# Performance work log

Hardware: AMD Instinct MI355X
Metric: run time of the kernel (lower is better)

## Reference

```python
import jax, jax.numpy as jnp
import numpy as np

D_MODEL = 1024
N_HEADS = 16
D_K = D_MODEL // N_HEADS
D_FF = 4096
EPS = 1e-6
NEG = -1e9


def layer_norm(x, alpha, bias):
    # torch: mean/std over last dim, std is unbiased (ddof=1), eps added to std
    mean = jnp.mean(x, axis=-1, keepdims=True)
    std = jnp.std(x, axis=-1, keepdims=True, ddof=1)
    return alpha * (x - mean) / (std + EPS) + bias


def setup_inputs() -> dict:
    key = jax.random.key(0)
    ks = jax.random.split(key, 12)
    B, S = 2, 2048
    s_attn = 1.0 / np.sqrt(D_MODEL)
    s_ff1 = 1.0 / np.sqrt(D_MODEL)
    s_ff2 = 1.0 / np.sqrt(D_FF)
    inp = {
        "x": jax.random.normal(ks[0], (B, S, D_MODEL), jnp.float32),
        "mask": jnp.ones((1, 1, S, S), jnp.int32),
        "wq": jax.random.normal(ks[1], (D_MODEL, D_MODEL), jnp.float32) * s_attn,
        "bq": jnp.zeros((D_MODEL,), jnp.float32),
        "wk": jax.random.normal(ks[2], (D_MODEL, D_MODEL), jnp.float32) * s_attn,
        "bk": jnp.zeros((D_MODEL,), jnp.float32),
        "wv": jax.random.normal(ks[3], (D_MODEL, D_MODEL), jnp.float32) * s_attn,
        "bv": jnp.zeros((D_MODEL,), jnp.float32),
        "wo": jax.random.normal(ks[4], (D_MODEL, D_MODEL), jnp.float32) * s_attn,
        "bo": jnp.zeros((D_MODEL,), jnp.float32),
        "w1": jax.random.normal(ks[5], (D_MODEL, D_FF), jnp.float32) * s_ff1,
        "b1": jnp.zeros((D_FF,), jnp.float32),
        "w2": jax.random.normal(ks[6], (D_FF, D_MODEL), jnp.float32) * s_ff2,
        "b2": jnp.zeros((D_MODEL,), jnp.float32),
        "a1": jnp.ones((1,), jnp.float32),
        "c1": jnp.zeros((1,), jnp.float32),
        "a2": jnp.ones((1,), jnp.float32),
        "c2": jnp.zeros((1,), jnp.float32),
    }
    return inp


def reference(x, mask, wq, bq, wk, bk, wv, bv, wo, bo, w1, b1, w2, b2, a1, c1, a2, c2):
    B, S, D = x.shape

    def mha(h):
        q = (h @ wq + bq).reshape(B, S, N_HEADS, D_K).transpose(0, 2, 1, 3)
        k = (h @ wk + bk).reshape(B, S, N_HEADS, D_K).transpose(0, 2, 1, 3)
        v = (h @ wv + bv).reshape(B, S, N_HEADS, D_K).transpose(0, 2, 1, 3)
        scores = jnp.einsum('bhqd,bhkd->bhqk', q, k) / jnp.sqrt(jnp.float32(D_K))
        scores = jnp.where(mask == 0, jnp.float32(NEG), scores)
        weights = jax.nn.softmax(scores, axis=-1)
        out = jnp.einsum('bhqk,bhkd->bhqd', weights, v)
        out = out.transpose(0, 2, 1, 3).reshape(B, S, D)
        return out @ wo + bo

    def ffn(h):
        return jax.nn.relu(h @ w1 + b1) @ w2 + b2

    # pre-LN residual connections (dropout=0 / eval mode)
    x = x + mha(layer_norm(x, a1, c1))
    x = x + ffn(layer_norm(x, a2, c2))
    return x
```

## Files before the change

### kernel.cpp

```cpp
#include <hip/hip_runtime.h>
#include <hip/hip_bf16.h>
#include <type_traits>


typedef __attribute__((ext_vector_type(8))) short short8v;
typedef __attribute__((ext_vector_type(4))) float f32x4;
typedef __attribute__((ext_vector_type(4))) unsigned uint4v;

#define D_MODEL 1024
#define SEQ 2048
#define NROWS 4096

__device__ __forceinline__ short f2bs(float f) {
  __hip_bfloat16 h = __float2bfloat16(f);
  return __builtin_bit_cast(short, h);
}

__device__ __forceinline__ unsigned cvtpk(float lo, float hi) {
  unsigned r;
  asm("v_cvt_pk_bf16_f32 %0, %1, %2" : "=v"(r) : "v"(lo), "v"(hi));
  return r;
}

__device__ __forceinline__ void perm16swap(unsigned& a, unsigned& b) {
  asm volatile("v_permlane16_swap_b32 %0, %1" : "+v"(a), "+v"(b));
}

__device__ __forceinline__ void async_copy16(const void* g, void* l) {
  __builtin_amdgcn_global_load_lds(
      (__attribute__((address_space(1))) void*)g,
      (__attribute__((address_space(3))) void*)l,
      16, 0, 0);
}

__global__ __launch_bounds__(256)
void transpose_bf16_kernel(const float* __restrict__ in, short* __restrict__ out,
                           int K, int N, float scale) {
  __shared__ float tile[32][33];
  const int n0 = blockIdx.x * 32, k0 = blockIdx.y * 32;
  const int tx = threadIdx.x, ty = threadIdx.y;
#pragma unroll
  for (int j = 0; j < 4; ++j)
    tile[ty + j * 8][tx] = in[(size_t)(k0 + ty + j * 8) * N + n0 + tx];
  __syncthreads();
#pragma unroll
  for (int j = 0; j < 4; ++j)
    out[(size_t)(n0 + ty + j * 8) * K + k0 + tx] = f2bs(tile[tx][ty + j * 8] * scale);
}

__global__ __launch_bounds__(256)
void transpose_v_kernel(const short* __restrict__ qkv, short* __restrict__ vt) {
  __shared__ short tile[32][33];
  const int bh = blockIdx.z, b = bh >> 4, h = bh & 15;
  const int s0 = blockIdx.x * 32, d0 = blockIdx.y * 32;
  const int tx = threadIdx.x, ty = threadIdx.y;
  const short* src = qkv + ((size_t)b * SEQ) * 3072 + 2048 + h * 64;
#pragma unroll
  for (int j = 0; j < 4; ++j)
    tile[ty + j * 8][tx] = src[(size_t)(s0 + ty + j * 8) * 3072 + d0 + tx];
  __syncthreads();
  short* dst = vt + (size_t)bh * 64 * SEQ;
#pragma unroll
  for (int j = 0; j < 4; ++j)
    dst[(size_t)(d0 + ty + j * 8) * SEQ + s0 + tx] = tile[tx][ty + j * 8];
}

__global__ void concat_bias_kernel(const float* __restrict__ bq, const float* __restrict__ bk,
                                   const float* __restrict__ bv, float* __restrict__ outb,
                                   float qscale) {
  int i = blockIdx.x * 256 + threadIdx.x;
  float v = (i < 1024) ? bq[i] * qscale : (i < 2048 ? bk[i - 1024] : bv[i - 2048]);
  outb[i] = v;
}

__global__ __launch_bounds__(256)
void layernorm_kernel(const float* __restrict__ x, short* __restrict__ out,
                      const float* __restrict__ alpha, const float* __restrict__ beta) {
  const int row = blockIdx.x;
  const int t = threadIdx.x;
  float4 v = ((const float4*)(x + (size_t)row * D_MODEL))[t];
  float s = v.x + v.y + v.z + v.w;
  float sq = v.x * v.x + v.y * v.y + v.z * v.z + v.w * v.w;
#pragma unroll
  for (int m = 1; m < 64; m <<= 1) {
    s += __shfl_xor(s, m, 64);
    sq += __shfl_xor(sq, m, 64);
  }
  __shared__ float sh_s[4], sh_q[4];
  const int wid = t >> 6;
  if ((t & 63) == 0) { sh_s[wid] = s; sh_q[wid] = sq; }
  __syncthreads();
  s = sh_s[0] + sh_s[1] + sh_s[2] + sh_s[3];
  sq = sh_q[0] + sh_q[1] + sh_q[2] + sh_q[3];
  const float mean = s * (1.0f / 1024.0f);
  const float var = fmaxf(0.0f, (sq - 1024.0f * mean * mean) * (1.0f / 1023.0f));
  const float scl = alpha[0] / (sqrtf(var) + 1e-6f);
  const float sft = beta[0];
  short4 o;
  o.x = f2bs((v.x - mean) * scl + sft);
  o.y = f2bs((v.y - mean) * scl + sft);
  o.z = f2bs((v.z - mean) * scl + sft);
  o.w = f2bs((v.w - mean) * scl + sft);
  ((short4*)(out + (size_t)row * D_MODEL))[t] = o;
}

template <int MF, int NF, bool RELU, bool RESID, bool OUT_BF16>
__global__ __launch_bounds__(256)
void gemm_bt_k64_kernel(const short* __restrict__ A, const short* __restrict__ Bt,
                        const float* __restrict__ bias, const float* __restrict__ resid,
                        void* __restrict__ out, int M, int N, int K) {
  constexpr int BM = MF * 32, BN = NF * 32, BK = 64;
  constexpr int ACH = BM * 8, BCH = BN * 8;
  __shared__ short As[2][BM * BK];
  __shared__ short Bs[2][BN * BK];
  const int tid = threadIdx.x;
  const int lane = tid & 63, wid = tid >> 6;
  const int wr = wid >> 1, wc = wid & 1;
  const int l15 = lane & 15, kg = lane >> 4;

  const int gx = gridDim.x;
  const int nwg = gx * gridDim.y;
  const int bid = blockIdx.y * gx + blockIdx.x;
  const int tilei = (bid & 7) * (nwg >> 3) + (bid >> 3);
  const int m0 = (tilei / gx) * BM, n0 = (tilei % gx) * BN;

  f32x4 acc[MF][NF];
#pragma unroll
  for (int m = 0; m < MF; ++m)
#pragma unroll
    for (int n = 0; n < NF; ++n) acc[m][n] = (f32x4){0.f, 0.f, 0.f, 0.f};

  auto stage = [&](int buf, int k0) {
#pragma unroll
    for (int it = 0; it < (ACH + BCH) / 256; ++it) {
      const int ch = tid + it * 256;
      if (ch < ACH) {
        const int r = ch >> 3, c = ch & 7;
        async_copy16(A + (size_t)(m0 + r) * K + k0 + ((c ^ (r & 7)) << 3),
                     &As[buf][ch * 8]);
      } else {
        const int cb = ch - ACH;
        const int r = cb >> 3, c = cb & 7;
        async_copy16(Bt + (size_t)(n0 + r) * K + k0 + ((c ^ (r & 7)) << 3),
                     &Bs[buf][cb * 8]);
      }
    }
  };

  stage(0, 0);
  __syncthreads();
  const int NT = K / BK;
  int buf = 0;
  for (int t = 0; t < NT; ++t) {
    if (t + 1 < NT) stage(buf ^ 1, (t + 1) * BK);
    short8v a[2][MF], b[2][NF];
#pragma unroll
    for (int m = 0; m < MF; ++m) {
      const int row = wr * MF * 16 + m * 16 + l15;
#pragma unroll
      for (int kt = 0; kt < 2; ++kt)
        a[kt][m] = *(const short8v*)&As[buf][row * BK + (((kg + 4 * kt) ^ (row & 7)) << 3)];
    }
#pragma unroll
    for (int n = 0; n < NF; ++n) {
      const int row = wc * NF * 16 + n * 16 + l15;
#pragma unroll
      for (int kt = 0; kt < 2; ++kt)
        b[kt][n] = *(const short8v*)&Bs[buf][row * BK + (((kg + 4 * kt) ^ (row & 7)) << 3)];
    }
    __builtin_amdgcn_s_setprio(1);
#pragma unroll
    for (int kt = 0; kt < 2; ++kt)
#pragma unroll
      for (int m = 0; m < MF; ++m)
#pragma unroll
        for (int n = 0; n < NF; ++n)
          acc[m][n] = __builtin_amdgcn_mfma_f32_16x16x32_bf16(a[kt][m], b[kt][n], acc[m][n], 0, 0, 0);
    __builtin_amdgcn_s_setprio(0);
    __syncthreads();
    buf ^= 1;
  }

#pragma unroll
  for (int m = 0; m < MF; ++m) {
#pragma unroll
    for (int n = 0; n < NF; ++n) {
      const int col = n0 + wc * NF * 16 + n * 16 + l15;
      const float bv = bias[col];
#pragma unroll
      for (int r = 0; r < 4; ++r) {
        const size_t row = (size_t)(m0 + wr * MF * 16 + m * 16 + kg * 4 + r);
        float v = acc[m][n][r] + bv;
        if (RELU) v = fmaxf(v, 0.0f);
        if (RESID) v += resid[row * N + col];
        if (OUT_BF16)
          ((short*)out)[row * N + col] = f2bs(v);
        else
          ((float*)out)[row * N + col] = v;
      }
    }
  }
}

__global__ __launch_bounds__(256)
void attn_kernel(const short* __restrict__ qkv, const short* __restrict__ vt,
                 short* __restrict__ out) {
  const int bh = blockIdx.y;
  const int b = bh >> 4, h = bh & 15;
  const int q0 = blockIdx.x * 64;
  const int tid = threadIdx.x;
  const int lane = tid & 63, wid = tid >> 6;
  const int l15 = lane & 15, kg = lane >> 4;

  __shared__ short Ks[2][64 * 64];
  __shared__ short Vs[2][64 * 64];

  const size_t RS = 3072;
  const short* Qb = qkv + (size_t)b * SEQ * RS + h * 64;
  const short* Kb = Qb + 1024;
  const short* Vtb = vt + (size_t)bh * 64 * SEQ;

  short8v qf[2];
  {
    const short* qrow = Qb + (size_t)(q0 + wid * 16 + l15) * RS + kg * 8;
    qf[0] = *(const short8v*)(qrow);
    qf[1] = *(const short8v*)(qrow + 32);
  }

  const int i0 = tid, i1 = tid + 256;
  const int r0 = i0 >> 3, b0 = (i0 & 7) ^ (r0 & 7);
  const int r1 = i1 >> 3, b1 = (i1 & 7) ^ (r1 & 7);

  auto stage = [&](int buf, int kv0) {
    async_copy16(Kb + (size_t)(kv0 + r0) * RS + b0 * 8, &Ks[buf][i0 * 8]);
    async_copy16(Kb + (size_t)(kv0 + r1) * RS + b1 * 8, &Ks[buf][i1 * 8]);
    async_copy16(Vtb + (size_t)r0 * SEQ + kv0 + b0 * 8, &Vs[buf][i0 * 8]);
    async_copy16(Vtb + (size_t)r1 * SEQ + kv0 + b1 * 8, &Vs[buf][i1 * 8]);
  };

  f32x4 o[4];
#pragma unroll
  for (int i = 0; i < 4; ++i) o[i] = (f32x4){0.f, 0.f, 0.f, 0.f};
  float lsum = 0.f;

  const int colblk = ((kg & 1) << 1) | (kg >> 1);

  auto tilebody = [&](auto BUFC, int kv_next, bool do_stage) {
    constexpr int buf = decltype(BUFC)::value;
    if (do_stage) stage(buf ^ 1, kv_next);

    f32x4 s[4];
    __builtin_amdgcn_s_setprio(1);
#pragma unroll
    for (int nt = 0; nt < 4; ++nt) {
      const int r = l15 + nt * 16, rx = r & 7;
      f32x4 c = (f32x4){0.f, 0.f, 0.f, 0.f};
      c = __builtin_amdgcn_mfma_f32_16x16x32_bf16(
          *(const short8v*)&Ks[buf][r * 64 + ((kg ^ rx) << 3)], qf[0], c, 0, 0, 0);
      c = __builtin_amdgcn_mfma_f32_16x16x32_bf16(
          *(const short8v*)&Ks[buf][r * 64 + (((kg + 4) ^ rx) << 3)], qf[1], c, 0, 0, 0);
      s[nt] = c;
    }
    __builtin_amdgcn_s_setprio(0);

    unsigned w[4][2];
#pragma unroll
    for (int nt = 0; nt < 4; ++nt) {
      float p0 = exp2f(s[nt][0]), p1 = exp2f(s[nt][1]);
      float p2 = exp2f(s[nt][2]), p3 = exp2f(s[nt][3]);
      lsum += (p0 + p1) + (p2 + p3);
      w[nt][0] = cvtpk(p0, p1);
      w[nt][1] = cvtpk(p2, p3);
    }

    __builtin_amdgcn_s_setprio(1);
#pragma unroll
    for (int kt = 0; kt < 2; ++kt) {
      unsigned x0 = w[2 * kt][0], y0 = w[2 * kt + 1][0];
      unsigned x1 = w[2 * kt][1], y1 = w[2 * kt + 1][1];
      perm16swap(x0, y0);
      perm16swap(x1, y1);
      uint4v uv = {x0, x1, y0, y1};
      short8v pf = __builtin_bit_cast(short8v, uv);
#pragma unroll
      for (int nt = 0; nt < 4; ++nt) {
        const int r = l15 + nt * 16;
        short8v vf = *(const short8v*)&Vs[buf][r * 64 + (((colblk + 4 * kt) ^ (r & 7)) << 3)];
        o[nt] = __builtin_amdgcn_mfma_f32_16x16x32_bf16(vf, pf, o[nt], 0, 0, 0);
      }
    }
    __builtin_amdgcn_s_setprio(0);

    __syncthreads();
  };

  stage(0, 0);
  __syncthreads();
  for (int kv0 = 0; kv0 < SEQ; kv0 += 128) {
    tilebody(std::integral_constant<int, 0>{}, kv0 + 64, true);
    tilebody(std::integral_constant<int, 1>{}, kv0 + 128, kv0 + 128 < SEQ);
  }

  lsum += __shfl_xor(lsum, 16, 64);
  lsum += __shfl_xor(lsum, 32, 64);
  const float linv = 1.0f / lsum;

  short* ob = out + ((size_t)b * SEQ + q0 + wid * 16 + l15) * D_MODEL + h * 64;
#pragma unroll
  for (int nt = 0; nt < 4; ++nt) {
    short4 st;
    st.x = f2bs(o[nt][0] * linv);
    st.y = f2bs(o[nt][1] * linv);
    st.z = f2bs(o[nt][2] * linv);
    st.w = f2bs(o[nt][3] * linv);
    *(short4*)(ob + nt * 16 + kg * 4) = st;
  }
}

static constexpr size_t OFF_WQKV = 0;
static constexpr size_t OFF_WO   = 6291456;
static constexpr size_t OFF_W1   = 8388608;
static constexpr size_t OFF_W2   = 16777216;
static constexpr size_t OFF_BQKV = 25165824;
static constexpr size_t OFF_H1   = 25178112;
static constexpr size_t OFF_QKV  = 33566720;
static constexpr size_t OFF_AO   = 58732544;
static constexpr size_t OFF_H2   = 67121152;
static constexpr size_t OFF_F1   = 75509760;
static constexpr size_t OFF_VT   = OFF_H1;

extern "C" void kernel_launch(void* const* d_in, const int* in_sizes, int n_in,
                              void* d_out, int out_size, void* d_ws, size_t ws_size,
                              hipStream_t stream) {
  const float* x  = (const float*)d_in[0];
  const float* wq = (const float*)d_in[2];
  const float* bq = (const float*)d_in[3];
  const float* wk = (const float*)d_in[4];
  const float* bk = (const float*)d_in[5];
  const float* wv = (const float*)d_in[6];
  const float* bv = (const float*)d_in[7];
  const float* wo = (const float*)d_in[8];
  const float* bo = (const float*)d_in[9];
  const float* w1 = (const float*)d_in[10];
  const float* b1 = (const float*)d_in[11];
  const float* w2 = (const float*)d_in[12];
  const float* b2 = (const float*)d_in[13];
  const float* a1 = (const float*)d_in[14];
  const float* c1 = (const float*)d_in[15];
  const float* a2 = (const float*)d_in[16];
  const float* c2 = (const float*)d_in[17];
  float* outp = (float*)d_out;
  char* ws = (char*)d_ws;

  short* wqkv_t = (short*)(ws + OFF_WQKV);
  short* wo_t   = (short*)(ws + OFF_WO);
  short* w1_t   = (short*)(ws + OFF_W1);
  short* w2_t   = (short*)(ws + OFF_W2);
  float* bqkv   = (float*)(ws + OFF_BQKV);
  short* h1     = (short*)(ws + OFF_H1);
  short* qkv    = (short*)(ws + OFF_QKV);
  short* ao     = (short*)(ws + OFF_AO);
  short* h2     = (short*)(ws + OFF_H2);
  short* f1     = (short*)(ws + OFF_F1);
  short* vtb    = (short*)(ws + OFF_VT);

  const float QSCALE = 0.125f * 1.44269504f;
  const dim3 tb(32, 8);
  transpose_bf16_kernel<<<dim3(32, 32), tb, 0, stream>>>(wq, wqkv_t, 1024, 1024, QSCALE);
  transpose_bf16_kernel<<<dim3(32, 32), tb, 0, stream>>>(wk, wqkv_t + (size_t)1024 * 1024, 1024, 1024, 1.0f);
  transpose_bf16_kernel<<<dim3(32, 32), tb, 0, stream>>>(wv, wqkv_t + (size_t)2048 * 1024, 1024, 1024, 1.0f);
  transpose_bf16_kernel<<<dim3(32, 32), tb, 0, stream>>>(wo, wo_t, 1024, 1024, 1.0f);
  transpose_bf16_kernel<<<dim3(128, 32), tb, 0, stream>>>(w1, w1_t, 1024, 4096, 1.0f);
  transpose_bf16_kernel<<<dim3(32, 128), tb, 0, stream>>>(w2, w2_t, 4096, 1024, 1.0f);
  concat_bias_kernel<<<12, 256, 0, stream>>>(bq, bk, bv, bqkv, QSCALE);

  layernorm_kernel<<<NROWS, 256, 0, stream>>>(x, h1, a1, c1);
  gemm_bt_k64_kernel<4, 2, false, false, true><<<dim3(48, 32), 256, 0, stream>>>(
      h1, wqkv_t, bqkv, nullptr, qkv, NROWS, 3072, 1024);
  transpose_v_kernel<<<dim3(64, 2, 32), tb, 0, stream>>>(qkv, vtb);
  attn_kernel<<<dim3(32, 32), 256, 0, stream>>>(qkv, vtb, ao);
  gemm_bt_k64_kernel<2, 2, false, true, false><<<dim3(16, 64), 256, 0, stream>>>(
      ao, wo_t, bo, x, d_out, NROWS, 1024, 1024);

  layernorm_kernel<<<NROWS, 256, 0, stream>>>(outp, h2, a2, c2);
  gemm_bt_k64_kernel<4, 2, true, false, true><<<dim3(64, 32), 256, 0, stream>>>(
      h2, w1_t, b1, nullptr, f1, NROWS, 4096, 1024);
  gemm_bt_k64_kernel<2, 2, false, true, false><<<dim3(16, 64), 256, 0, stream>>>(
      f1, w2_t, b2, outp, d_out, NROWS, 1024, 4096);
}
```

Baseline: 266.6 us.

## Use single-buffered 128x128 GEMM for QKV/FFN1 and MFMA row-sum in attention

Adds a single-buffered GEMM kernel with 128x128 tiles and uses it for the QKV and FFN1 projections. The larger tiles give more operand reuse per block, at the cost of no double buffering and fewer blocks in the grid. In attention, the softmax denominator is now computed with an extra MFMA against a vector of ones, replacing the scalar adds and cross-lane shuffles. Separately, exp2f is swapped for the hardware exp2 builtin. The row sum is now accumulated from bf16-rounded probabilities, which slightly changes numerics.

```diff
diff --git a/kernel.cpp b/kernel.cpp
--- a/kernel.cpp
+++ b/kernel.cpp
@@ -106,6 +106,95 @@
 
 template <int MF, int NF, bool RELU, bool RESID, bool OUT_BF16>
 __global__ __launch_bounds__(256)
+void gemm_bt_sb_kernel(const short* __restrict__ A, const short* __restrict__ Bt,
+                       const float* __restrict__ bias, const float* __restrict__ resid,
+                       void* __restrict__ out, int M, int N, int K) {
+  constexpr int BM = MF * 32, BN = NF * 32, BK = 64;
+  __shared__ short As[BM * BK];
+  __shared__ short Bs[BN * BK];
+  const int tid = threadIdx.x;
+  const int lane = tid & 63, wid = tid >> 6;
+  const int wr = wid >> 1, wc = wid & 1;
+  const int l15 = lane & 15, kg = lane >> 4;
+
+  const int gx = gridDim.x;
+  const int nwg = gx * gridDim.y;
+  const int bid = blockIdx.y * gx + blockIdx.x;
+  const int tilei = (bid & 7) * (nwg >> 3) + (bid >> 3);
+  const int m0 = (tilei / gx) * BM, n0 = (tilei % gx) * BN;
+
+  f32x4 acc[MF][NF];
+#pragma unroll
+  for (int m = 0; m < MF; ++m)
+#pragma unroll
+    for (int n = 0; n < NF; ++n) acc[m][n] = (f32x4){0.f, 0.f, 0.f, 0.f};
+
+  const int r0 = tid >> 3, c0 = tid & 7;
+  const int csw = (c0 ^ (r0 & 7)) << 3;
+  const short* pa = A + (size_t)(m0 + r0) * K + csw;
+  const short* pb = Bt + (size_t)(n0 + r0) * K + csw;
+
+  const int NT = K / BK;
+  for (int t = 0; t < NT; ++t) {
+    const size_t ko = (size_t)t * BK;
+#pragma unroll
+    for (int it = 0; it < MF; ++it)
+      async_copy16(pa + (size_t)it * 32 * K + ko, &As[(tid + it * 256) * 8]);
+#pragma unroll
+    for (int it = 0; it < NF; ++it)
+      async_copy16(pb + (size_t)it * 32 * K + ko, &Bs[(tid + it * 256) * 8]);
+    __syncthreads();
+
+    short8v a[2][MF], b[2][NF];
+#pragma unroll
+    for (int m = 0; m < MF; ++m) {
+      const int row = wr * MF * 16 + m * 16 + l15;
+#pragma unroll
+      for (int kt = 0; kt < 2; ++kt)
+        a[kt][m] = *(const short8v*)&As[row * BK + (((kg + 4 * kt) ^ (row & 7)) << 3)];
+    }
+#pragma unroll
+    for (int n = 0; n < NF; ++n) {
+      const int row = wc * NF * 16 + n * 16 + l15;
+#pragma unroll
+      for (int kt = 0; kt < 2; ++kt)
+        b[kt][n] = *(const short8v*)&Bs[row * BK + (((kg + 4 * kt) ^ (row & 7)) << 3)];
+    }
+    __builtin_amdgcn_s_setprio(1);
+#pragma unroll
+    for (int kt = 0; kt < 2; ++kt)
+#pragma unroll
+      for (int m = 0; m < MF; ++m)
+#pragma unroll
+        for (int n = 0; n < NF; ++n)
+          acc[m][n] = __builtin_amdgcn_mfma_f32_16x16x32_bf16(a[kt][m], b[kt][n], acc[m][n], 0, 0, 0);
+    __builtin_amdgcn_s_setprio(0);
+    __syncthreads();
+  }
+
+#pragma unroll
+  for (int m = 0; m < MF; ++m) {
+#pragma unroll
+    for (int n = 0; n < NF; ++n) {
+      const int col = n0 + wc * NF * 16 + n * 16 + l15;
+      const float bv = bias[col];
+#pragma unroll
+      for (int r = 0; r < 4; ++r) {
+        const size_t row = (size_t)(m0 + wr * MF * 16 + m * 16 + kg * 4 + r);
+        float v = acc[m][n][r] + bv;
+        if (RELU) v = fmaxf(v, 0.0f);
+        if (RESID) v += resid[row * N + col];
+        if (OUT_BF16)
+          ((short*)out)[row * N + col] = f2bs(v);
+        else
+          ((float*)out)[row * N + col] = v;
+      }
+    }
+  }
+}
+
+template <int MF, int NF, bool RELU, bool RESID, bool OUT_BF16>
+__global__ __launch_bounds__(256)
 void gemm_bt_k64_kernel(const short* __restrict__ A, const short* __restrict__ Bt,
                         const float* __restrict__ bias, const float* __restrict__ resid,
                         void* __restrict__ out, int M, int N, int K) {
@@ -241,7 +330,10 @@
   f32x4 o[4];
 #pragma unroll
   for (int i = 0; i < 4; ++i) o[i] = (f32x4){0.f, 0.f, 0.f, 0.f};
-  float lsum = 0.f;
+  f32x4 lacc = (f32x4){0.f, 0.f, 0.f, 0.f};
+
+  const short ONE = 0x3F80;
+  const short8v ones = {ONE, ONE, ONE, ONE, ONE, ONE, ONE, ONE};
 
   const int colblk = ((kg & 1) << 1) | (kg >> 1);
 
@@ -266,9 +358,10 @@
     unsigned w[4][2];
 #pragma unroll
     for (int nt = 0; nt < 4; ++nt) {
-      float p0 = exp2f(s[nt][0]), p1 = exp2f(s[nt][1]);
-      float p2 = exp2f(s[nt][2]), p3 = exp2f(s[nt][3]);
-      lsum += (p0 + p1) + (p2 + p3);
+      float p0 = __builtin_amdgcn_exp2f(s[nt][0]);
+      float p1 = __builtin_amdgcn_exp2f(s[nt][1]);
+      float p2 = __builtin_amdgcn_exp2f(s[nt][2]);
+      float p3 = __builtin_amdgcn_exp2f(s[nt][3]);
       w[nt][0] = cvtpk(p0, p1);
       w[nt][1] = cvtpk(p2, p3);
     }
@@ -282,6 +375,7 @@
       perm16swap(x1, y1);
       uint4v uv = {x0, x1, y0, y1};
       short8v pf = __builtin_bit_cast(short8v, uv);
+      lacc = __builtin_amdgcn_mfma_f32_16x16x32_bf16(ones, pf, lacc, 0, 0, 0);
 #pragma unroll
       for (int nt = 0; nt < 4; ++nt) {
         const int r = l15 + nt * 16;
@@ -301,9 +395,7 @@
     tilebody(std::integral_constant<int, 1>{}, kv0 + 128, kv0 + 128 < SEQ);
   }
 
-  lsum += __shfl_xor(lsum, 16, 64);
-  lsum += __shfl_xor(lsum, 32, 64);
-  const float linv = 1.0f / lsum;
+  const float linv = 1.0f / lacc[0];
 
   short* ob = out + ((size_t)b * SEQ + q0 + wid * 16 + l15) * D_MODEL + h * 64;
 #pragma unroll
@@ -375,7 +467,7 @@
   concat_bias_kernel<<<12, 256, 0, stream>>>(bq, bk, bv, bqkv, QSCALE);
 
   layernorm_kernel<<<NROWS, 256, 0, stream>>>(x, h1, a1, c1);
-  gemm_bt_k64_kernel<4, 2, false, false, true><<<dim3(48, 32), 256, 0, stream>>>(
+  gemm_bt_sb_kernel<4, 4, false, false, true><<<dim3(24, 32), 256, 0, stream>>>(
       h1, wqkv_t, bqkv, nullptr, qkv, NROWS, 3072, 1024);
   transpose_v_kernel<<<dim3(64, 2, 32), tb, 0, stream>>>(qkv, vtb);
   attn_kernel<<<dim3(32, 32), 256, 0, stream>>>(qkv, vtb, ao);
@@ -383,7 +475,7 @@
       ao, wo_t, bo, x, d_out, NROWS, 1024, 1024);
 
   layernorm_kernel<<<NROWS, 256, 0, stream>>>(outp, h2, a2, c2);
-  gemm_bt_k64_kernel<4, 2, true, false, true><<<dim3(64, 32), 256, 0, stream>>>(
+  gemm_bt_sb_kernel<4, 4, true, false, true><<<dim3(32, 32), 256, 0, stream>>>(
       h2, w1_t, b1, nullptr, f1, NROWS, 4096, 1024);
   gemm_bt_k64_kernel<2, 2, false, true, false><<<dim3(16, 64), 256, 0, stream>>>(
       f1, w2_t, b2, outp, d_out, NROWS, 1024, 4096);
```

After: 241.1 us. 9.6% less time.
